# Kernel optimization log

Hardware: AMD Instinct MI355X
Metric: run time of the kernel (lower is better)

## Reference

```python
import jax, jax.numpy as jnp
import numpy as np

PS = 8; STRIDE = 1; NVALS = 31
DELTA = 0.05; ETA = 0.01; TAU = 0.1
B = 2; CIN = 32; H = 64; W = 64
HP = (H - PS) // STRIDE + 1
WP = (W - PS) // STRIDE + 1
TWO_PI = 2.0 * np.pi

# patch-local coordinate grid (torch.meshgrid 'ij': y varies along rows)
_lin = np.linspace(-1.0, 1.0, PS).astype(np.float32)
YG = jnp.asarray(np.tile(_lin[:, None], (1, PS)))[None, :, :, None, None]  # [1,ps,ps,1,1]
XG = jnp.asarray(np.tile(_lin[None, :], (PS, 1)))[None, :, :, None, None]

ANGLE_RANGE = jnp.asarray(np.linspace(0.0, TWO_PI, NVALS + 1, dtype=np.float32)[:NVALS])
XY_RANGE = jnp.asarray(np.linspace(-3.0, 3.0, NVALS, dtype=np.float32))

# unfold/fold index maps: pixel (hp*stride + px, wp*stride + py)
RI = jnp.arange(PS)[:, None] + STRIDE * jnp.arange(HP)[None, :]  # [ps,hp]
CI = jnp.arange(PS)[:, None] + STRIDE * jnp.arange(WP)[None, :]  # [ps,wp]
R4 = RI[:, None, :, None]  # [ps,1,hp,1]
C4 = CI[None, :, None, :]  # [1,ps,1,wp]


def conv1x1(x, w):
    return jnp.einsum('bchw,oc->bohw', x, w)


def bn(x, gamma, beta, eps=1e-5):
    # BatchNorm2d in training mode: batch statistics, biased variance
    m = x.mean(axis=(0, 2, 3), keepdims=True)
    v = x.var(axis=(0, 2, 3), keepdims=True)
    return gamma[None, :, None, None] * (x - m) * jax.lax.rsqrt(v + eps) + beta[None, :, None, None]


def silu(x):
    return x * jax.nn.sigmoid(x)


def params_to_distances(params):
    # params: [n,5,hp,wp] -> dists [n,2,ps,ps,hp,wp]
    x0 = params[:, 3][:, None, None]  # [n,1,1,hp,wp]
    y0 = params[:, 4][:, None, None]
    ang = jnp.sort(jnp.mod(params[:, :3], TWO_PI), axis=1)
    a1 = ang[:, 0][:, None, None]
    a2 = ang[:, 1][:, None, None]
    a3 = ang[:, 2][:, None, None]
    a4 = 0.5 * (a1 + a3) + jnp.where(jnp.mod(0.5 * (a1 - a3), TWO_PI) >= np.pi, np.pi, 0.0)

    def g(dt):
        return (dt / np.pi - 1.0) ** 35

    def line(a):
        return -jnp.sin(a) * (XG - x0) + jnp.cos(a) * (YG - y0)

    d42 = jnp.mod(a2 - a4, TWO_PI)
    sgn42 = jnp.where(d42 < np.pi, 1.0, -1.0)
    dist42 = sgn42 * jnp.minimum(sgn42 * line(a4), -sgn42 * line(a2)) + g(d42) * TAU
    d13 = jnp.mod(a3 - a1, TWO_PI)
    sgn13 = jnp.where(d13 < np.pi, 1.0, -1.0)
    dist13 = sgn13 * jnp.minimum(sgn13 * line(a1), -sgn13 * line(a3)) + g(d13) * TAU
    return jnp.stack([dist13, dist42], axis=1)


def wedges_of(dists):
    hd = 0.5 * (1.0 + (2.0 / np.pi) * jnp.arctan(dists / ETA))
    h0, h1 = hd[:, 0], hd[:, 1]
    return jnp.stack([1.0 - h0, h0 * (1.0 - h1), h0 * h1], axis=1)  # [n,3,ps,ps,hp,wp]


def dcp(params, imgp):
    # params [n,5,hp,wp], imgp [c,ps,ps,hp,wp]
    dists = params_to_distances(params)
    w = wedges_of(dists)
    wsum = w.sum(axis=(2, 3))  # [n,3,hp,wp]
    cnum = jnp.einsum('cxyHW,nkxyHW->nckHW', imgp, w)
    colors = cnum / (wsum[:, None] + 1e-10)  # [n,c,3,hp,wp]
    patches = jnp.einsum('nkxyHW,nckHW->ncxyHW', w, colors)
    return dists, colors, patches


def boundaries_of(dists):
    d1, d2 = dists[:, 0:1], dists[:, 1:2]
    mad = jnp.where(d1 < 0.0, -d1,
                    jnp.where(d2 < 0.0, jnp.minimum(d1, -d2), jnp.minimum(d1, d2)))
    return 1.0 / (1.0 + (mad / DELTA) ** 2)


def fold(patches):
    # [B,C,ps,ps,hp,wp] -> [B,C,H,W] (sum over overlapping patches)
    Bn, C = patches.shape[:2]
    return jnp.zeros((Bn, C, H, W), patches.dtype).at[:, :, R4, C4].add(patches)


def forward(x, reduce_w, reduce_gamma, reduce_beta, fb_w, fb_gamma, fb_beta, fi_w, fi_gamma, fi_beta):
    xr = silu(bn(conv1x1(x, reduce_w), reduce_gamma, reduce_beta))  # [B,3,H,W]
    imgp = xr[:, :, R4, C4]  # unfold -> [B,3,ps,ps,hp,wp]
    num_patches = jnp.zeros((H, W), xr.dtype).at[R4, C4].add(
        jnp.ones((PS, PS, HP, WP), xr.dtype))

    params = jnp.zeros((x.shape[0], 5, HP, WP), xr.dtype)

    def make_step(i, prange):
        def step(p_b, imgp_b):
            pq = jnp.repeat(p_b[None], NVALS, axis=0)  # [n,5,hp,wp]
            pq = pq.at[:, i].add(prange[:, None, None])
            _, _, patches = dcp(pq, imgp_b)
            loss = ((imgp_b[None] - patches) ** 2).mean(axis=(2, 3)).sum(axis=1)  # [n,hp,wp]
            best = jnp.argmin(loss, axis=0)
            vals = jnp.take_along_axis(pq[:, i], best[None], axis=0)[0]
            return p_b.at[i].set(vals)
        return step

    for i in range(5):  # coordinate descent over 3 angles then x0, y0
        prange = ANGLE_RANGE if i < 3 else XY_RANGE
        params = jax.vmap(make_step(i, prange))(params, imgp)

    def finalize(p_b, imgp_b):
        dists, _, patches = dcp(p_b[None], imgp_b)
        return patches[0], boundaries_of(dists)[0]

    patches_all, lb_all = jax.vmap(finalize)(params, imgp)
    smoothed = fold(patches_all) / num_patches[None, None]  # [B,3,H,W]
    gb = fold(lb_all) / num_patches[None, None]             # [B,1,H,W]
    gb3 = jnp.broadcast_to(gb, (gb.shape[0], 3, H, W))
    boundaries = silu(bn(conv1x1(gb3, fb_w), fb_gamma, fb_beta))
    image = silu(bn(conv1x1(smoothed, fi_w), fi_gamma, fi_beta))
    return boundaries, image


def setup_inputs() -> dict:
    key = jax.random.key(0)
    ks = jax.random.split(key, 4)
    return {
        'x': jax.random.normal(ks[0], (B, CIN, H, W), jnp.float32),
        'reduce_w': jax.random.normal(ks[1], (3, CIN), jnp.float32) * 0.1,
        'reduce_gamma': jnp.ones((3,), jnp.float32),
        'reduce_beta': jnp.zeros((3,), jnp.float32),
        'fb_w': jax.random.normal(ks[2], (1, 3), jnp.float32) * 0.3,
        'fb_gamma': jnp.ones((1,), jnp.float32),
        'fb_beta': jnp.zeros((1,), jnp.float32),
        'fi_w': jax.random.normal(ks[3], (1, 3), jnp.float32) * 0.3,
        'fi_gamma': jnp.ones((1,), jnp.float32),
        'fi_beta': jnp.zeros((1,), jnp.float32),
    }


def reference(x, reduce_w, reduce_gamma, reduce_beta, fb_w, fb_gamma, fb_beta, fi_w, fi_gamma, fi_beta):
    return forward(x, reduce_w, reduce_gamma, reduce_beta, fb_w, fb_gamma, fb_beta, fi_w, fi_gamma, fi_beta)
```

## Files before the change

### kernel.cpp

```cpp
#include <hip/hip_runtime.h>
#include <math.h>

#define B_    2
#define CIN_  32
#define H_    64
#define W_    64
#define HP_   57
#define WP_   57
#define NP_   (B_*HP_*WP_)
#define NVALS_ 31

#define XR_OFF   0
#define FP_OFF   24576
#define FG_OFF   49152
#define ST_OFF   57344
#define WS_TOTAL 57360

static __device__ __forceinline__ float mod2pi(float x) {
    const float TP = (float)(2.0 * M_PI);
    float m = fmodf(x, TP);
    return (m < 0.0f) ? (m + TP) : m;
}
static __device__ __forceinline__ float pow35f(float t) {
    float t2 = t * t, t4 = t2 * t2, t8 = t4 * t4, t16 = t8 * t8, t32 = t16 * t16;
    return t32 * t2 * t;
}
static __device__ __forceinline__ float siluf(float x) {
    return x / (1.0f + expf(-x));
}
static __device__ __forceinline__ float wave_sum(float v) {
#pragma unroll
    for (int m = 1; m < 64; m <<= 1) v += __shfl_xor(v, m);
    return v;
}
static __device__ __forceinline__ float lin_of(int k) {
    return (float)(-1.0 + (double)k * (2.0 / 7.0));
}

static __device__ __forceinline__ float fast_atan(float x) {
    const float PIO2 = 1.5707963267948966f;
    const float PIO4 = 0.7853981633974483f;
    const float T3P8 = 2.414213562373095f;
    const float TP8  = 0.41421356237309503f;
    float ax = fabsf(x);
    bool big = ax > T3P8;
    bool mid = ax > TP8;
    float denom = big ? ax : (ax + 1.0f);
    float r = __builtin_amdgcn_rcpf(denom);
    float zr = big ? -r : (ax - 1.0f) * r;
    float z  = mid ? zr : ax;
    float y0 = big ? PIO2 : (mid ? PIO4 : 0.0f);
    float z2 = z * z;
    float p = fmaf(fmaf(fmaf(8.05374449538e-2f, z2, -1.38776856032e-1f),
                        z2, 1.99777106478e-1f),
                   z2, -3.33329491539e-1f);
    float res = fmaf(p * z2, z, z);
    return copysignf(y0 + res, x);
}

struct Geo {
    float X1, Y1, X3, Y3;
    float X4, Y4, X2, Y2;
    float sgn13, sgn42, g13, g42, x0, y0;
};

static __device__ void setup_geo(float p0, float p1, float p2, float p3, float p4,
                                 Geo& G) {
    const float PIF = (float)M_PI;
    float m0 = mod2pi(p0), m1 = mod2pi(p1), m2 = mod2pi(p2);
    float lo = fminf(m0, m1), hi = fmaxf(m0, m1);
    float a1 = fminf(lo, m2);
    float a3 = fmaxf(hi, m2);
    float a2 = fmaxf(fminf(hi, m2), lo);
    float hm = mod2pi(0.5f * (a1 - a3));
    float a4 = 0.5f * (a1 + a3) + ((hm >= PIF) ? PIF : 0.0f);
    float d42 = mod2pi(a2 - a4);
    G.sgn42 = (d42 < PIF) ? 1.0f : -1.0f;
    G.g42 = pow35f(d42 / PIF - 1.0f) * 0.1f;
    float d13 = mod2pi(a3 - a1);
    G.sgn13 = (d13 < PIF) ? 1.0f : -1.0f;
    G.g13 = pow35f(d13 / PIF - 1.0f) * 0.1f;
    float s1 = sinf(a1), c1 = cosf(a1);
    float s2 = sinf(a2), c2 = cosf(a2);
    float s3 = sinf(a3), c3 = cosf(a3);
    float s4 = sinf(a4), c4 = cosf(a4);
    G.X1 = -G.sgn13 * s1;  G.Y1 =  G.sgn13 * c1;
    G.X3 =  G.sgn13 * s3;  G.Y3 = -G.sgn13 * c3;
    G.X4 = -G.sgn42 * s4;  G.Y4 =  G.sgn42 * c4;
    G.X2 =  G.sgn42 * s2;  G.Y2 = -G.sgn42 * c2;
    G.x0 = p3; G.y0 = p4;
}

static __device__ __forceinline__ void dists_at(const Geo& G, float xg, float yg,
                                                float& d13, float& d42) {
    float dx = xg - G.x0, dy = yg - G.y0;
    float u1 = G.X1 * dx + G.Y1 * dy;
    float u3 = G.X3 * dx + G.Y3 * dy;
    float u4 = G.X4 * dx + G.Y4 * dy;
    float u2 = G.X2 * dx + G.Y2 * dy;
    d13 = G.sgn13 * fminf(u1, u3) + G.g13;
    d42 = G.sgn42 * fminf(u4, u2) + G.g42;
}

static __device__ __forceinline__ void wedge_of(float d13, float d42,
                                                float& w0, float& w1, float& w2) {
    const float C1OPI = 0.3183098861837907f;
    float hd0 = fmaf(C1OPI, fast_atan(d13 * 100.0f), 0.5f);
    float hd1 = fmaf(C1OPI, fast_atan(d42 * 100.0f), 0.5f);
    w0 = 1.0f - hd0;
    w1 = hd0 * (1.0f - hd1);
    w2 = hd0 * hd1;
}

__global__ __launch_bounds__(128) void head_in_conv(const float* __restrict__ x,
                                                    const float* __restrict__ rw,
                                                    float* __restrict__ xr,
                                                    float* __restrict__ st) {
    const int e = blockIdx.x * 128 + threadIdx.x;
    const int b = e >> 12, rem = e & 4095;
    const float* xp = x + (size_t)b * CIN_ * 4096 + rem;
    float a0 = 0.0f, a1 = 0.0f, a2 = 0.0f;
#pragma unroll
    for (int c = 0; c < CIN_; ++c) {
        float xv = xp[c * 4096];
        a0 += rw[c] * xv;
        a1 += rw[32 + c] * xv;
        a2 += rw[64 + c] * xv;
    }
    xr[(b * 3 + 0) * 4096 + rem] = a0;
    xr[(b * 3 + 1) * 4096 + rem] = a1;
    xr[(b * 3 + 2) * 4096 + rem] = a2;
    float s0 = wave_sum(a0), q0 = wave_sum(a0 * a0);
    float s1 = wave_sum(a1), q1 = wave_sum(a1 * a1);
    float s2 = wave_sum(a2), q2 = wave_sum(a2 * a2);
    if ((threadIdx.x & 63) == 0) {
        atomicAdd(&st[0], s0); atomicAdd(&st[1], s1); atomicAdd(&st[2], s2);
        atomicAdd(&st[3], q0); atomicAdd(&st[4], q1); atomicAdd(&st[5], q2);
    }
}

__global__ __launch_bounds__(128) void mega_kernel(const float* __restrict__ xr,
                                                   const float* __restrict__ gamma,
                                                   const float* __restrict__ beta,
                                                   const float* __restrict__ st,
                                                   float* __restrict__ foldP,
                                                   float* __restrict__ foldG) {
    __shared__ float s_img[2][192];
    __shared__ float s_lin[8];
    const int t = threadIdx.x;
    if (t < 8) s_lin[t] = lin_of(t);
    const int lg = t >> 6, lane = t & 63;
    const int patch = blockIdx.x * 2 + lg;
    const bool active = (patch < NP_);
    int b = 0, hp = 0, wp = 0;
    if (active) {
        b = patch / (HP_ * WP_);
        int pi = patch - b * (HP_ * WP_);
        hp = pi / WP_; wp = pi - hp * WP_;
        const int pr = lane >> 3, pc = lane & 7;
        const int goff = ((hp + pr) << 6) + (wp + pc);
#pragma unroll
        for (int c = 0; c < 3; ++c) {
            float mean = st[c] / 8192.0f;
            float var  = st[3 + c] / 8192.0f - mean * mean;
            float sc = gamma[c] / sqrtf(var + 1e-5f);
            float sh = beta[c] - mean * sc;
            float v  = xr[((b * 3 + c) << 12) + goff];
            s_img[lg][64 * c + lane] = siluf(v * sc + sh);
        }
    }
    __syncthreads();
    if (!active) return;

    const int cand = lane >> 1;
    const int half = lane & 1;
    const float* img = s_img[lg] + half * 32;
    const int yoff = half << 2;

    float p0 = 0.0f, p1 = 0.0f, p2 = 0.0f, p3 = 0.0f, p4 = 0.0f;

#pragma unroll 1
    for (int step = 0; step < 5; ++step) {
        const float base = (step == 0) ? p0 : (step == 1) ? p1 :
                           (step == 2) ? p2 : (step == 3) ? p3 : p4;
        const int ci = (cand < NVALS_) ? cand : (NVALS_ - 1);
        float add;
        if (step < 3) add = (float)((double)ci * (6.283185307179586476925286766559 / 31.0));
        else          add = (float)(-3.0 + (double)ci * 0.2);
        const float pv = base + add;
        Geo G;
        setup_geo((step == 0) ? pv : p0, (step == 1) ? pv : p1,
                  (step == 2) ? pv : p2, (step == 3) ? pv : p3,
                  (step == 4) ? pv : p4, G);

        float ws0 = 0, ws1 = 0;
        float is0 = 0, is1 = 0, is2 = 0;
        float cn00 = 0, cn01 = 0, cn10 = 0, cn11 = 0, cn20 = 0, cn21 = 0;
        float g00 = 0, g01 = 0, g11 = 0;
#pragma unroll 1
        for (int r = 0; r < 4; ++r) {
            const float yg = s_lin[yoff + r];
            const float dy = yg - G.y0;
            const float t1 = G.Y1 * dy, t3 = G.Y3 * dy;
            const float t4 = G.Y4 * dy, t2 = G.Y2 * dy;
#pragma unroll
            for (int cth = 0; cth < 8; ++cth) {
                const int i = r * 8 + cth;
                const float dx = s_lin[cth] - G.x0;
                float u1 = G.X1 * dx + t1;
                float u3 = G.X3 * dx + t3;
                float u4 = G.X4 * dx + t4;
                float u2 = G.X2 * dx + t2;
                float d13 = G.sgn13 * fminf(u1, u3) + G.g13;
                float d42 = G.sgn42 * fminf(u4, u2) + G.g42;
                float w0, w1, w2;
                wedge_of(d13, d42, w0, w1, w2);
                float i0 = img[i], i1 = img[64 + i], i2 = img[128 + i];
                ws0 += w0; ws1 += w1;
                is0 += i0; is1 += i1; is2 += i2;
                cn00 += i0 * w0; cn01 += i0 * w1;
                cn10 += i1 * w0; cn11 += i1 * w1;
                cn20 += i2 * w0; cn21 += i2 * w1;
                g00 += w0 * w0; g01 += w0 * w1; g11 += w1 * w1;
            }
        }
        ws0 += __shfl_xor(ws0, 1); ws1 += __shfl_xor(ws1, 1);
        is0 += __shfl_xor(is0, 1); is1 += __shfl_xor(is1, 1); is2 += __shfl_xor(is2, 1);
        cn00 += __shfl_xor(cn00, 1); cn01 += __shfl_xor(cn01, 1);
        cn10 += __shfl_xor(cn10, 1); cn11 += __shfl_xor(cn11, 1);
        cn20 += __shfl_xor(cn20, 1); cn21 += __shfl_xor(cn21, 1);
        g00 += __shfl_xor(g00, 1); g01 += __shfl_xor(g01, 1); g11 += __shfl_xor(g11, 1);

        float ws2  = 64.0f - ws0 - ws1;
        float cn02 = is0 - cn00 - cn01;
        float cn12 = is1 - cn10 - cn11;
        float cn22 = is2 - cn20 - cn21;
        float g02  = ws0 - g00 - g01;
        float g12  = ws1 - g01 - g11;
        float g22  = ws2 - g02 - g12;

        float r0 = 1.0f / (ws0 + 1e-10f);
        float r1 = 1.0f / (ws1 + 1e-10f);
        float r2 = 1.0f / (ws2 + 1e-10f);
        float c00 = cn00 * r0, c01 = cn01 * r1, c02 = cn02 * r2;
        float c10 = cn10 * r0, c11 = cn11 * r1, c12 = cn12 * r2;
        float c20 = cn20 * r0, c21 = cn21 * r1, c22 = cn22 * r2;

        float loss =
            (c00 * c00 * g00 + c01 * c01 * g11 + c02 * c02 * g22
             + 2.0f * (c00 * c01 * g01 + c00 * c02 * g02 + c01 * c02 * g12)
             - 2.0f * (c00 * cn00 + c01 * cn01 + c02 * cn02))
          + (c10 * c10 * g00 + c11 * c11 * g11 + c12 * c12 * g22
             + 2.0f * (c10 * c11 * g01 + c10 * c12 * g02 + c11 * c12 * g12)
             - 2.0f * (c10 * cn10 + c11 * cn11 + c12 * cn12))
          + (c20 * c20 * g00 + c21 * c21 * g11 + c22 * c22 * g22
             + 2.0f * (c20 * c21 * g01 + c20 * c22 * g02 + c21 * c22 * g12)
             - 2.0f * (c20 * cn20 + c21 * cn21 + c22 * cn22));
        if (cand >= NVALS_) loss = INFINITY;

        float bl = loss; int bi = cand;
#pragma unroll
        for (int off = 32; off > 0; off >>= 1) {
            float ol = __shfl_down(bl, (unsigned)off);
            int   oi = __shfl_down(bi, (unsigned)off);
            if (ol < bl || (ol == bl && oi < bi)) { bl = ol; bi = oi; }
        }
        bi = __shfl(bi, 0);
        float badd;
        if (step < 3) badd = (float)((double)bi * (6.283185307179586476925286766559 / 31.0));
        else          badd = (float)(-3.0 + (double)bi * 0.2);
        const float bv = base + badd;
        if (step == 0) p0 = bv; else if (step == 1) p1 = bv;
        else if (step == 2) p2 = bv; else if (step == 3) p3 = bv; else p4 = bv;
    }

    {
        Geo G; setup_geo(p0, p1, p2, p3, p4, G);
        const int pr = lane >> 3, pc = lane & 7;
        float xg = s_lin[pc], yg = s_lin[pr];
        float d13, d42;
        dists_at(G, xg, yg, d13, d42);
        float w0, w1, w2;
        wedge_of(d13, d42, w0, w1, w2);
        float i0 = s_img[lg][lane];
        float i1 = s_img[lg][64 + lane];
        float i2 = s_img[lg][128 + lane];

        float r[12] = { w0, w1, w2,
                        i0 * w0, i0 * w1, i0 * w2,
                        i1 * w0, i1 * w1, i1 * w2,
                        i2 * w0, i2 * w1, i2 * w2 };
#pragma unroll
        for (int m = 1; m < 64; m <<= 1) {
#pragma unroll
            for (int j = 0; j < 12; ++j) r[j] += __shfl_xor(r[j], m);
        }
        float col[3][3];
#pragma unroll
        for (int c = 0; c < 3; ++c) {
            col[c][0] = r[3 + c * 3 + 0] / (r[0] + 1e-10f);
            col[c][1] = r[3 + c * 3 + 1] / (r[1] + 1e-10f);
            col[c][2] = r[3 + c * 3 + 2] / (r[2] + 1e-10f);
        }
        float o0 = w0 * col[0][0] + w1 * col[0][1] + w2 * col[0][2];
        float o1 = w0 * col[1][0] + w1 * col[1][1] + w2 * col[1][2];
        float o2 = w0 * col[2][0] + w1 * col[2][1] + w2 * col[2][2];

        float mad = (d13 < 0.0f) ? -d13 : ((d42 < 0.0f) ? fminf(d13, -d42) : fminf(d13, d42));
        float tt = mad / 0.05f;
        float lb = 1.0f / (1.0f + tt * tt);

        const int off = ((hp + pr) << 6) + (wp + pc);
        atomicAdd(&foldP[(b * 3 + 0) * 4096 + off], o0);
        atomicAdd(&foldP[(b * 3 + 1) * 4096 + off], o1);
        atomicAdd(&foldP[(b * 3 + 2) * 4096 + off], o2);
        atomicAdd(&foldG[b * 4096 + off], lb);
    }
}

static __device__ __forceinline__ float np_count(int tpos) {
    int lo = (tpos - 56 > 0) ? (tpos - 56) : 0;
    int hi = (tpos < 7) ? tpos : 7;
    return (float)(hi - lo + 1);
}

__global__ __launch_bounds__(1024) void head_out(const float* __restrict__ foldP,
                                                 const float* __restrict__ foldG,
                                                 const float* __restrict__ fb_w,
                                                 const float* __restrict__ fb_g,
                                                 const float* __restrict__ fb_b,
                                                 const float* __restrict__ fi_w,
                                                 const float* __restrict__ fi_g,
                                                 const float* __restrict__ fi_b,
                                                 float* __restrict__ out) {
    __shared__ float sB[8192];
    __shared__ float sI[8192];
    __shared__ float red[16][4];
    __shared__ float s_sc[4];
    const int t = threadIdx.x;
    float sb = 0, qb = 0, si = 0, qi = 0;
#pragma unroll
    for (int k = 0; k < 8; ++k) {
        const int e = t + 1024 * k;
        const int b = e >> 12, h = (e >> 6) & 63, w = e & 63;
        const float inv = 1.0f / (np_count(h) * np_count(w));
        float gv = foldG[e] * inv;
        float vb = fb_w[0] * gv + fb_w[1] * gv + fb_w[2] * gv;
        const int off = (h << 6) + w;
        float v0 = foldP[(b * 3 + 0) * 4096 + off] * inv;
        float v1 = foldP[(b * 3 + 1) * 4096 + off] * inv;
        float v2 = foldP[(b * 3 + 2) * 4096 + off] * inv;
        float vi = fi_w[0] * v0 + fi_w[1] * v1 + fi_w[2] * v2;
        sB[e] = vb; sI[e] = vi;
        sb += vb; qb += vb * vb; si += vi; qi += vi * vi;
    }
    sb = wave_sum(sb); qb = wave_sum(qb); si = wave_sum(si); qi = wave_sum(qi);
    const int wid = t >> 6;
    if ((t & 63) == 0) { red[wid][0] = sb; red[wid][1] = qb; red[wid][2] = si; red[wid][3] = qi; }
    __syncthreads();
    if (t == 0) {
        float S = 0, Q = 0, S2 = 0, Q2 = 0;
#pragma unroll
        for (int w = 0; w < 16; ++w) { S += red[w][0]; Q += red[w][1]; S2 += red[w][2]; Q2 += red[w][3]; }
        float meanB = S / 8192.0f,  varB = Q / 8192.0f - meanB * meanB;
        float meanI = S2 / 8192.0f, varI = Q2 / 8192.0f - meanI * meanI;
        float scB = fb_g[0] / sqrtf(varB + 1e-5f);
        float scI = fi_g[0] / sqrtf(varI + 1e-5f);
        s_sc[0] = scB; s_sc[1] = fb_b[0] - meanB * scB;
        s_sc[2] = scI; s_sc[3] = fi_b[0] - meanI * scI;
    }
    __syncthreads();
    const float scB = s_sc[0], shB = s_sc[1], scI = s_sc[2], shI = s_sc[3];
#pragma unroll
    for (int k = 0; k < 8; ++k) {
        const int e = t + 1024 * k;
        out[e]        = siluf(sB[e] * scB + shB);
        out[8192 + e] = siluf(sI[e] * scI + shI);
    }
}

extern "C" void kernel_launch(void* const* d_in, const int* in_sizes, int n_in,
                              void* d_out, int out_size, void* d_ws, size_t ws_size,
                              hipStream_t stream) {
    (void)in_sizes; (void)n_in; (void)out_size; (void)ws_size;
    const float* x        = (const float*)d_in[0];
    const float* reduce_w = (const float*)d_in[1];
    const float* reduce_g = (const float*)d_in[2];
    const float* reduce_b = (const float*)d_in[3];
    const float* fb_w     = (const float*)d_in[4];
    const float* fb_g     = (const float*)d_in[5];
    const float* fb_b     = (const float*)d_in[6];
    const float* fi_w     = (const float*)d_in[7];
    const float* fi_g     = (const float*)d_in[8];
    const float* fi_b     = (const float*)d_in[9];
    float* ws     = (float*)d_ws;
    float* xr     = ws + XR_OFF;
    float* foldP  = ws + FP_OFF;
    float* foldG  = ws + FG_OFF;
    float* st     = ws + ST_OFF;
    float* out    = (float*)d_out;

    hipMemsetAsync(foldP, 0, (size_t)(WS_TOTAL - FP_OFF) * sizeof(float), stream);

    head_in_conv<<<64, 128, 0, stream>>>(x, reduce_w, xr, st);
    mega_kernel<<<(NP_ + 1) / 2, 128, 0, stream>>>(xr, reduce_g, reduce_b, st,
                                                   foldP, foldG);
    head_out<<<1, 1024, 0, stream>>>(foldP, foldG, fb_w, fb_g, fb_b,
                                     fi_w, fi_g, fi_b, out);
}
```

Baseline: 261.1 us.

## Fold zeroing into input conv, hoist image sums, use 4 patches per block

The fold buffers are now zeroed inside head_in_conv, so the large memset shrinks to a small stats-only memset. The per-patch image channel sums are computed once before the search loop instead of on every step. mega_kernel now runs four patches per 256-thread block. The custom fast_atan is also replaced with library atanf, which is likely more accurate but costs more per call in the inner wedge loop.

```diff
diff --git a/kernel.cpp b/kernel.cpp
--- a/kernel.cpp
+++ b/kernel.cpp
@@ -35,27 +35,6 @@
 }
 static __device__ __forceinline__ float lin_of(int k) {
     return (float)(-1.0 + (double)k * (2.0 / 7.0));
-}
-
-static __device__ __forceinline__ float fast_atan(float x) {
-    const float PIO2 = 1.5707963267948966f;
-    const float PIO4 = 0.7853981633974483f;
-    const float T3P8 = 2.414213562373095f;
-    const float TP8  = 0.41421356237309503f;
-    float ax = fabsf(x);
-    bool big = ax > T3P8;
-    bool mid = ax > TP8;
-    float denom = big ? ax : (ax + 1.0f);
-    float r = __builtin_amdgcn_rcpf(denom);
-    float zr = big ? -r : (ax - 1.0f) * r;
-    float z  = mid ? zr : ax;
-    float y0 = big ? PIO2 : (mid ? PIO4 : 0.0f);
-    float z2 = z * z;
-    float p = fmaf(fmaf(fmaf(8.05374449538e-2f, z2, -1.38776856032e-1f),
-                        z2, 1.99777106478e-1f),
-                   z2, -3.33329491539e-1f);
-    float res = fmaf(p * z2, z, z);
-    return copysignf(y0 + res, x);
 }
 
 struct Geo {
@@ -104,9 +83,9 @@
 
 static __device__ __forceinline__ void wedge_of(float d13, float d42,
                                                 float& w0, float& w1, float& w2) {
-    const float C1OPI = 0.3183098861837907f;
-    float hd0 = fmaf(C1OPI, fast_atan(d13 * 100.0f), 0.5f);
-    float hd1 = fmaf(C1OPI, fast_atan(d42 * 100.0f), 0.5f);
+    const float C2OPI = (float)(2.0 / M_PI);
+    float hd0 = 0.5f * (1.0f + C2OPI * atanf(d13 * 100.0f));
+    float hd1 = 0.5f * (1.0f + C2OPI * atanf(d42 * 100.0f));
     w0 = 1.0f - hd0;
     w1 = hd0 * (1.0f - hd1);
     w2 = hd0 * hd1;
@@ -115,8 +94,10 @@
 __global__ __launch_bounds__(128) void head_in_conv(const float* __restrict__ x,
                                                     const float* __restrict__ rw,
                                                     float* __restrict__ xr,
-                                                    float* __restrict__ st) {
+                                                    float* __restrict__ st,
+                                                    float4* __restrict__ foldZ) {
     const int e = blockIdx.x * 128 + threadIdx.x;
+    foldZ[e] = make_float4(0.0f, 0.0f, 0.0f, 0.0f);
     const int b = e >> 12, rem = e & 4095;
     const float* xp = x + (size_t)b * CIN_ * 4096 + rem;
     float a0 = 0.0f, a1 = 0.0f, a2 = 0.0f;
@@ -139,18 +120,18 @@
     }
 }
 
-__global__ __launch_bounds__(128) void mega_kernel(const float* __restrict__ xr,
+__global__ __launch_bounds__(256) void mega_kernel(const float* __restrict__ xr,
                                                    const float* __restrict__ gamma,
                                                    const float* __restrict__ beta,
                                                    const float* __restrict__ st,
                                                    float* __restrict__ foldP,
                                                    float* __restrict__ foldG) {
-    __shared__ float s_img[2][192];
+    __shared__ float s_img[4][192];
     __shared__ float s_lin[8];
     const int t = threadIdx.x;
     if (t < 8) s_lin[t] = lin_of(t);
     const int lg = t >> 6, lane = t & 63;
-    const int patch = blockIdx.x * 2 + lg;
+    const int patch = blockIdx.x * 4 + lg;
     const bool active = (patch < NP_);
     int b = 0, hp = 0, wp = 0;
     if (active) {
@@ -176,6 +157,13 @@
     const int half = lane & 1;
     const float* img = s_img[lg] + half * 32;
     const int yoff = half << 2;
+
+    float is0 = 0, is1 = 0, is2 = 0;
+#pragma unroll
+    for (int i = 0; i < 32; ++i) {
+        is0 += img[i]; is1 += img[64 + i]; is2 += img[128 + i];
+    }
+    is0 += __shfl_xor(is0, 1); is1 += __shfl_xor(is1, 1); is2 += __shfl_xor(is2, 1);
 
     float p0 = 0.0f, p1 = 0.0f, p2 = 0.0f, p3 = 0.0f, p4 = 0.0f;
 
@@ -194,7 +182,6 @@
                   (step == 4) ? pv : p4, G);
 
         float ws0 = 0, ws1 = 0;
-        float is0 = 0, is1 = 0, is2 = 0;
         float cn00 = 0, cn01 = 0, cn10 = 0, cn11 = 0, cn20 = 0, cn21 = 0;
         float g00 = 0, g01 = 0, g11 = 0;
 #pragma unroll 1
@@ -217,7 +204,6 @@
                 wedge_of(d13, d42, w0, w1, w2);
                 float i0 = img[i], i1 = img[64 + i], i2 = img[128 + i];
                 ws0 += w0; ws1 += w1;
-                is0 += i0; is1 += i1; is2 += i2;
                 cn00 += i0 * w0; cn01 += i0 * w1;
                 cn10 += i1 * w0; cn11 += i1 * w1;
                 cn20 += i2 * w0; cn21 += i2 * w1;
@@ -225,7 +211,6 @@
             }
         }
         ws0 += __shfl_xor(ws0, 1); ws1 += __shfl_xor(ws1, 1);
-        is0 += __shfl_xor(is0, 1); is1 += __shfl_xor(is1, 1); is2 += __shfl_xor(is2, 1);
         cn00 += __shfl_xor(cn00, 1); cn01 += __shfl_xor(cn01, 1);
         cn10 += __shfl_xor(cn10, 1); cn11 += __shfl_xor(cn11, 1);
         cn20 += __shfl_xor(cn20, 1); cn21 += __shfl_xor(cn21, 1);
@@ -400,10 +385,10 @@
     float* st     = ws + ST_OFF;
     float* out    = (float*)d_out;
 
-    hipMemsetAsync(foldP, 0, (size_t)(WS_TOTAL - FP_OFF) * sizeof(float), stream);
-
-    head_in_conv<<<64, 128, 0, stream>>>(x, reduce_w, xr, st);
-    mega_kernel<<<(NP_ + 1) / 2, 128, 0, stream>>>(xr, reduce_g, reduce_b, st,
+    hipMemsetAsync(st, 0, 16 * sizeof(float), stream);
+
+    head_in_conv<<<64, 128, 0, stream>>>(x, reduce_w, xr, st, (float4*)foldP);
+    mega_kernel<<<(NP_ + 3) / 4, 256, 0, stream>>>(xr, reduce_g, reduce_b, st,
                                                    foldP, foldG);
     head_out<<<1, 1024, 0, stream>>>(foldP, foldG, fb_w, fb_g, fb_b,
                                      fi_w, fi_g, fi_b, out);
```

Result: faster. 235.6 us (-9.8%).
